# Optimization experiments

Hardware: AMD Instinct MI355X
Metric: run time of the kernel (lower is better)

Reference implementation:

```python
import jax, jax.numpy as jnp
import numpy as np

N, D, K = 131072, 768, 2000


def setup_inputs() -> dict:
    key = jax.random.key(0)
    kx, kc = jax.random.split(key)
    x = jax.random.normal(kx, (N, D), dtype=jnp.float32)
    centroids = jax.random.normal(kc, (D, K), dtype=jnp.float32)  # stored as [D, K] like the torch module
    return {"x": x, "centroids": centroids}


def reference(x, centroids):
    # dist[n,k] = ||x_n||^2 - 2 x_n . c_k + ||c_k||^2  (matmul trick)
    x_norm = jnp.sum(x * x, axis=1, keepdims=True)              # [N, 1]
    c_norm = jnp.sum(centroids * centroids, axis=0, keepdims=True)  # [1, K]
    dist = x_norm - 2.0 * jnp.matmul(x, centroids) + c_norm     # [N, K]
    return jnp.argmin(dist, axis=-1)                            # [N] int
```

## Files before the change

### kernel.cpp

```cpp
#include <hip/hip_runtime.h>
#include <hip/hip_bf16.h>

#define N_ROWS 131072
#define DIM    768
#define K_C    2000
#define K_PAD  2048
#define TAU    0.2f
#define LISTCAP 8192

typedef _Float16 f16;
typedef _Float16 f16x4 __attribute__((ext_vector_type(4)));
typedef _Float16 f16x8 __attribute__((ext_vector_type(8)));
typedef float    f32x4 __attribute__((ext_vector_type(4)));

#define OFF_CN   6291456
#define OFF_XN   6299648
#define OFF_PMIN 6823936
#define OFF_PSEC 15212544
#define OFF_PIDX 23601152
#define OFF_CNT  31989760
#define OFF_LIST 31990016
#define OFF_CN64 32022784
#define OFF_XH   32039168

static __device__ __forceinline__ void gload16(const void* g, void* l) {
  __builtin_amdgcn_global_load_lds(
      (const __attribute__((address_space(1))) unsigned int*)g,
      (__attribute__((address_space(3))) unsigned int*)l, 16, 0, 0);
}

__global__ __launch_bounds__(256) void prep_cn(const float* __restrict__ cent,
                                               float* __restrict__ cn,
                                               double* __restrict__ cn64) {
#pragma clang fp contract(off)
  __shared__ float pf[8][32];
  __shared__ double pd[8][32];
  int t = threadIdx.x;
  int kk = t & 31;
  int k = blockIdx.x * 32 + kk;
  int p = t >> 5;
  float s = 0.0f;
  double s64 = 0.0;
  for (int d = p * 96; d < p * 96 + 96; ++d) {
    float c = (k < K_C) ? cent[d * K_C + k] : 0.0f;
    float sq = c * c;
    s = s + sq;
    s64 += (double)c * (double)c;
  }
  pf[p][kk] = s;
  pd[p][kk] = s64;
  __syncthreads();
  if (p == 0) {
    float ss = 0.0f;
    double ss64 = 0.0;
#pragma unroll
    for (int q = 0; q < 8; ++q) {
      ss = ss + pf[q][kk];
      ss64 += pd[q][kk];
    }
    cn[k] = (k < K_C) ? ss : INFINITY;
    cn64[k] = (k < K_C) ? ss64 : (double)INFINITY;
  }
}

__global__ __launch_bounds__(256) void prep_ct(const float* __restrict__ cent,
                                               f16* __restrict__ cTh) {
  __shared__ float ld[64][65];
  int k0 = blockIdx.x * 64;
  int d0 = blockIdx.y * 64;
  int tid = threadIdx.x;
#pragma unroll
  for (int it = 0; it < 16; ++it) {
    int idx = it * 256 + tid;
    int dd = idx >> 6, kk = idx & 63;
    int k = k0 + kk;
    ld[dd][kk] = (k < K_C) ? cent[(size_t)(d0 + dd) * K_C + k] : 0.0f;
  }
  __syncthreads();
#pragma unroll
  for (int it = 0; it < 16; ++it) {
    int idx = it * 256 + tid;
    int kk = idx >> 6, dd = idx & 63;
    cTh[(size_t)(k0 + kk) * DIM + d0 + dd] = (f16)ld[dd][kk];
  }
}

__global__ __launch_bounds__(256) void xnorm_prepx(const float* __restrict__ x,
                                                   float* __restrict__ xn,
                                                   f16* __restrict__ xh) {
#pragma clang fp contract(off)
  __shared__ __align__(16) float buf[16 * DIM];
  int row0 = blockIdx.x * 16;
  int tid = threadIdx.x;
  const f32x4* src = (const f32x4*)(x + (size_t)row0 * DIM);
  f32x4* dst = (f32x4*)buf;
#pragma unroll
  for (int c = 0; c < 12; ++c) {
    f32x4 v = src[c * 256 + tid];
    dst[c * 256 + tid] = v;
    f16x4 hv;
#pragma unroll
    for (int j = 0; j < 4; ++j) hv[j] = (f16)v[j];
    *(f16x4*)(xh + (size_t)row0 * DIM + (size_t)(c * 256 + tid) * 4) = hv;
  }
  __syncthreads();
  int w = tid >> 6, lane = tid & 63;
  int b = lane >> 3, j = lane & 7;
#pragma unroll
  for (int rr = 0; rr < 4; ++rr) {
    int r = w * 4 + rr;
    const float* a = buf + r * DIM + 96 * b + j;
    float v0 = a[0];
    float acc = v0 * v0;
#pragma unroll
    for (int t = 1; t < 12; ++t) {
      float q = a[8 * t];
      float s = q * q;
      acc = acc + s;
    }
    float v = acc;
    { float o = __shfl_xor(v, 1);  v = v + o; }
    { float o = __shfl_xor(v, 2);  v = v + o; }
    { float o = __shfl_xor(v, 4);  v = v + o; }
    { float o = __shfl_xor(v, 8);  v = v + o; }
    { float o = __shfl_xor(v, 16); v = v + o; }
    { float o = __shfl_xor(v, 32); v = v + o; }
    if (lane == 0) xn[row0 + r] = v;
  }
}

#define STAGE3(bufo)                                                           \
  do {                                                                         \
    gload16(pA0, ldsb + (bufo) + c0 * 1024);                                   \
    gload16(pA1, ldsb + (bufo) + c1 * 1024);                                   \
    gload16(pB0, ldsb + 24576 + (bufo) + c0 * 1024);                           \
    gload16(pB1, ldsb + 24576 + (bufo) + c1 * 1024);                           \
    pA0 += 64; pA1 += 64; pB0 += 64; pB1 += 64;                                \
  } while (0)

__global__ __launch_bounds__(256, 3) void kmeans_main(
    const f16* __restrict__ xh, const f16* __restrict__ cTh,
    const float* __restrict__ cn, const float* __restrict__ xn,
    float* __restrict__ pmin, float* __restrict__ psec,
    int* __restrict__ pidx) {
  __shared__ __align__(16) f16 lds[24576];
  char* ldsb = (char*)lds;

  int d0 = blockIdx.x;
  int g  = (d0 & 7) * 2048 + (d0 >> 3);
  int pb = g & 15;
  int rb = g >> 4;

  int tid  = threadIdx.x;
  int w    = tid >> 6;
  int lane = tid & 63;
  int wrow = (w >> 1) * 64;
  int wcol = (w & 1) * 64;

  int rsel = lane & 15;
  int ksel = lane >> 4;
  int rs = (ksel ^ ((rsel >> 1) & 3)) << 4;

  int c0 = w * 2, c1 = w * 2 + 1;
  int grn = (lane & 3) ^ ((lane >> 3) & 3);
  const char* pA0 = (const char*)xh +
      ((size_t)(rb * 128 + c0 * 16 + (lane >> 2)) * DIM + grn * 8) * 2;
  const char* pA1 = (const char*)xh +
      ((size_t)(rb * 128 + c1 * 16 + (lane >> 2)) * DIM + grn * 8) * 2;
  const char* pB0 = (const char*)cTh +
      ((size_t)(pb * 128 + c0 * 16 + (lane >> 2)) * DIM + grn * 8) * 2;
  const char* pB1 = (const char*)cTh +
      ((size_t)(pb * 128 + c1 * 16 + (lane >> 2)) * DIM + grn * 8) * 2;

  f32x4 acc[4][4] = {};

  STAGE3(0);
  STAGE3(8192);

  int cb = 0;
  int sb = 16384;
#pragma unroll 3
  for (int kt = 0; kt < 24; ++kt) {
    if (kt < 23) {
      asm volatile("s_waitcnt vmcnt(4)" ::: "memory");
    } else {
      asm volatile("s_waitcnt vmcnt(0)" ::: "memory");
    }
    __builtin_amdgcn_sched_barrier(0);
    __builtin_amdgcn_s_barrier();
    __builtin_amdgcn_sched_barrier(0);

    if (kt < 22) STAGE3(sb);

    f16x8 ah[4], bh[4];
    int abase = cb + (wrow + rsel) * 64 + rs;
    int bbase = cb + 24576 + (wcol + rsel) * 64 + rs;
#pragma unroll
    for (int m = 0; m < 4; ++m) ah[m] = *(const f16x8*)(ldsb + abase + m * 1024);
#pragma unroll
    for (int n = 0; n < 4; ++n) bh[n] = *(const f16x8*)(ldsb + bbase + n * 1024);

    __builtin_amdgcn_s_setprio(1);
#pragma unroll
    for (int m = 0; m < 4; ++m)
#pragma unroll
      for (int n = 0; n < 4; ++n)
        acc[m][n] = __builtin_amdgcn_mfma_f32_16x16x32_f16(ah[m], bh[n],
                                                           acc[m][n], 0, 0, 0);
    __builtin_amdgcn_s_setprio(0);

    cb = (cb == 16384) ? 0 : cb + 8192;
    sb = (sb == 16384) ? 0 : sb + 8192;
  }

  __syncthreads();
  float* lv = (float*)lds;
  float* lsv = (float*)lds + 256;
  int*   li = (int*)((float*)lds + 512);

  int colbase = pb * 128 + wcol + rsel;
  float cnv[4];
#pragma unroll
  for (int n = 0; n < 4; ++n) cnv[n] = cn[colbase + n * 16];
  int g4 = ksel * 4;

#pragma unroll
  for (int m = 0; m < 4; ++m) {
#pragma unroll
    for (int j = 0; j < 4; ++j) {
      int trow = wrow + m * 16 + g4 + j;
      float xv = xn[rb * 128 + trow];
      float v1 = 0.0f, v2 = INFINITY;
      int i1 = 0;
#pragma unroll
      for (int n = 0; n < 4; ++n) {
        float dd = (xv - 2.0f * acc[m][n][j]) + cnv[n];
        int ci = colbase + n * 16;
        if (n == 0) { v1 = dd; i1 = ci; }
        else if (dd < v1) { v2 = v1; v1 = dd; i1 = ci; }
        else { v2 = fminf(v2, dd); }
      }
#pragma unroll
      for (int off = 1; off < 16; off <<= 1) {
        float ov1 = __shfl_xor(v1, off);
        float ov2 = __shfl_xor(v2, off);
        int oi1 = __shfl_xor(i1, off);
        if (ov1 < v1 || (ov1 == v1 && oi1 < i1)) {
          v2 = fminf(v1, ov2); v1 = ov1; i1 = oi1;
        } else {
          v2 = fminf(v2, ov1);
        }
      }
      if ((lane & 15) == 0) {
        lv[(w & 1) * 128 + trow] = v1;
        lsv[(w & 1) * 128 + trow] = v2;
        li[(w & 1) * 128 + trow] = i1;
      }
    }
  }
  __syncthreads();
  if (tid < 128) {
    float a1 = lv[tid], a2 = lsv[tid];
    int aj = li[tid];
    float b1 = lv[128 + tid], b2 = lsv[128 + tid];
    int bj = li[128 + tid];
    float v1, v2; int i1;
    if (b1 < a1 || (b1 == a1 && bj < aj)) { v1 = b1; i1 = bj; v2 = fminf(b2, a1); }
    else { v1 = a1; i1 = aj; v2 = fminf(a2, b1); }
    size_t o = (size_t)pb * N_ROWS + rb * 128 + tid;
    pmin[o] = v1;
    psec[o] = v2;
    pidx[o] = i1;
  }
}

__global__ void merge_detect(const float* __restrict__ pmin,
                             const float* __restrict__ psec,
                             const int* __restrict__ pidx, int* __restrict__ out,
                             int* __restrict__ list, int* __restrict__ counter) {
  int n = blockIdx.x * 256 + threadIdx.x;
  float v1 = INFINITY, v2 = INFINITY;
  int i1 = 0x7fffffff;
  for (int p = 0; p < 16; ++p) {
    float a1 = pmin[(size_t)p * N_ROWS + n];
    float a2 = psec[(size_t)p * N_ROWS + n];
    int aj = pidx[(size_t)p * N_ROWS + n];
    if (a1 < v1 || (a1 == v1 && aj < i1)) {
      v2 = fminf(v1, a2); v1 = a1; i1 = aj;
    } else {
      v2 = fminf(v2, a1);
    }
  }
  out[n] = i1;
  if (v2 - v1 < TAU) {
    int idx = atomicAdd(counter, 1);
    if (idx < LISTCAP) list[idx] = n;
  }
}

#define ACCS(R) \
  double a##R##0 = 0, a##R##1 = 0, a##R##2 = 0, a##R##3 = 0, \
         a##R##4 = 0, a##R##5 = 0, a##R##6 = 0, a##R##7 = 0
#define FMAS(R, XV) \
  a##R##0 = fma(XV, c0, a##R##0); a##R##1 = fma(XV, c1, a##R##1); \
  a##R##2 = fma(XV, c2, a##R##2); a##R##3 = fma(XV, c3, a##R##3); \
  a##R##4 = fma(XV, c4, a##R##4); a##R##5 = fma(XV, c5, a##R##5); \
  a##R##6 = fma(XV, c6, a##R##6); a##R##7 = fma(XV, c7, a##R##7)
#define EVAL(R)                                                         \
  {                                                                     \
    double dots[8] = {a##R##0, a##R##1, a##R##2, a##R##3,               \
                      a##R##4, a##R##5, a##R##6, a##R##7};              \
    double bv = (double)INFINITY;                                       \
    int bi = 0x7fffffff;                                                \
    _Pragma("unroll") for (int j = 0; j < 8; ++j) {                     \
      int k = tid + j * 256;                                            \
      if (k < K_C) {                                                    \
        double dd = (xnorms[R] - 2.0 * dots[j]) + cn64[k];              \
        if (dd < bv) { bv = dd; bi = k; }                               \
      }                                                                 \
    }                                                                   \
    rv[tid] = bv; ri[tid] = bi;                                         \
    __syncthreads();                                                    \
    for (int s = 128; s > 0; s >>= 1) {                                 \
      if (tid < s) {                                                    \
        double ov = rv[tid + s];                                        \
        int oi = ri[tid + s];                                           \
        if (ov < rv[tid] || (ov == rv[tid] && oi < ri[tid])) {          \
          rv[tid] = ov; ri[tid] = oi;                                   \
        }                                                               \
      }                                                                 \
      __syncthreads();                                                  \
    }                                                                   \
    if (tid == 0 && (R) < nrows) out[list[b0 + (R)]] = ri[0];           \
    __syncthreads();                                                    \
  }

__global__ __launch_bounds__(256) void exact_recheck64(
    const float* __restrict__ x, const float* __restrict__ cent,
    const double* __restrict__ cn64, const int* __restrict__ list,
    const int* __restrict__ counter, int* __restrict__ out) {
  __shared__ __align__(16) float xrow[4][DIM];
  __shared__ double rv[256];
  __shared__ int ri[256];
  __shared__ double xnorms[4];
  int cnt = counter[0];
  if (cnt > LISTCAP) cnt = LISTCAP;
  int b0 = blockIdx.x * 4;
  if (b0 >= cnt) return;
  int nrows = cnt - b0;
  if (nrows > 4) nrows = 4;
  int tid = threadIdx.x;
  for (int r = 0; r < 4; ++r) {
    int n = list[b0 + (r < nrows ? r : 0)];
    double part = 0.0;
    for (int d = tid; d < DIM; d += 256) {
      float v = x[(size_t)n * DIM + d];
      xrow[r][d] = v;
      part += (double)v * (double)v;
    }
    rv[tid] = part;
    __syncthreads();
    for (int s = 128; s > 0; s >>= 1) {
      if (tid < s) rv[tid] += rv[tid + s];
      __syncthreads();
    }
    if (tid == 0) xnorms[r] = rv[0];
    __syncthreads();
  }

  int k7 = tid + 1792;
  int k7c = (k7 < K_C) ? k7 : (K_C - 1);
  ACCS(0); ACCS(1); ACCS(2); ACCS(3);
#pragma unroll 2
  for (int d = 0; d < DIM; ++d) {
    const float* cp = cent + (size_t)d * K_C + tid;
    double c0 = cp[0], c1 = cp[256], c2 = cp[512], c3 = cp[768];
    double c4 = cp[1024], c5 = cp[1280], c6 = cp[1536];
    double c7 = cp[k7c - tid];
    double x0 = xrow[0][d], x1 = xrow[1][d];
    double x2 = xrow[2][d], x3 = xrow[3][d];
    FMAS(0, x0); FMAS(1, x1); FMAS(2, x2); FMAS(3, x3);
  }
  EVAL(0) EVAL(1) EVAL(2) EVAL(3)
}

extern "C" void kernel_launch(void* const* d_in, const int* in_sizes, int n_in,
                              void* d_out, int out_size, void* d_ws, size_t ws_size,
                              hipStream_t stream) {
  const float* x = (const float*)d_in[0];
  const float* cent = (const float*)d_in[1];
  char* ws = (char*)d_ws;
  f16* cTh = (f16*)ws;
  float* cn = (float*)(ws + OFF_CN);
  float* xn = (float*)(ws + OFF_XN);
  float* pmin = (float*)(ws + OFF_PMIN);
  float* psec = (float*)(ws + OFF_PSEC);
  int* pidx = (int*)(ws + OFF_PIDX);
  int* counter = (int*)(ws + OFF_CNT);
  int* list = (int*)(ws + OFF_LIST);
  double* cn64 = (double*)(ws + OFF_CN64);
  f16* xh = (f16*)(ws + OFF_XH);

  hipMemsetAsync(counter, 0, 4, stream);
  prep_cn<<<64, 256, 0, stream>>>(cent, cn, cn64);
  prep_ct<<<dim3(32, 12), 256, 0, stream>>>(cent, cTh);
  xnorm_prepx<<<N_ROWS / 16, 256, 0, stream>>>(x, xn, xh);
  kmeans_main<<<16384, 256, 0, stream>>>(xh, cTh, cn, xn, pmin, psec, pidx);
  merge_detect<<<N_ROWS / 256, 256, 0, stream>>>(pmin, psec, pidx, (int*)d_out,
                                                 list, counter);
  exact_recheck64<<<LISTCAP / 4, 256, 0, stream>>>(x, cent, cn64, list, counter,
                                                   (int*)d_out);
}
```

Measured before the change: 1.098 ms.

## Widen GEMM block tile to 128x256 with 8x4 MFMA tiles per wave

Each block now computes a 128-row by 256-centroid tile, with every wave covering all 128 rows and its own 64 centroids, in place of a 128x128 tile. This halves the grid and the number of partial-min slabs the merge kernel reads, and raises operand reuse per LDS load. In exchange, per-block LDS and accumulator registers double (launch bounds drop to 2 blocks per CU), which lowers occupancy. The cross-wave merge now drops the index tie-break and uses an odd second-min update.

Result: slower. 1.166 ms (+6.1%).

```diff
diff --git a/kernel.cpp b/kernel.cpp
--- a/kernel.cpp
+++ b/kernel.cpp
@@ -131,58 +131,62 @@
 
 #define STAGE3(bufo)                                                           \
   do {                                                                         \
-    gload16(pA0, ldsb + (bufo) + c0 * 1024);                                   \
-    gload16(pA1, ldsb + (bufo) + c1 * 1024);                                   \
-    gload16(pB0, ldsb + 24576 + (bufo) + c0 * 1024);                           \
-    gload16(pB1, ldsb + 24576 + (bufo) + c1 * 1024);                           \
-    pA0 += 64; pA1 += 64; pB0 += 64; pB1 += 64;                                \
+    gload16(pA0, ldsb + (bufo) + (w * 2) * 1024);                              \
+    gload16(pA1, ldsb + (bufo) + (w * 2 + 1) * 1024);                          \
+    gload16(pB0, ldsb + (bufo) + 8192 + (w * 4) * 1024);                       \
+    gload16(pB1, ldsb + (bufo) + 8192 + (w * 4 + 1) * 1024);                   \
+    gload16(pB2, ldsb + (bufo) + 8192 + (w * 4 + 2) * 1024);                   \
+    gload16(pB3, ldsb + (bufo) + 8192 + (w * 4 + 3) * 1024);                   \
+    pA0 += 64; pA1 += 64; pB0 += 64; pB1 += 64; pB2 += 64; pB3 += 64;          \
   } while (0)
 
-__global__ __launch_bounds__(256, 3) void kmeans_main(
+__global__ __launch_bounds__(256, 2) void kmeans_main(
     const f16* __restrict__ xh, const f16* __restrict__ cTh,
     const float* __restrict__ cn, const float* __restrict__ xn,
     float* __restrict__ pmin, float* __restrict__ psec,
     int* __restrict__ pidx) {
-  __shared__ __align__(16) f16 lds[24576];
+  __shared__ __align__(16) f16 lds[36864];
   char* ldsb = (char*)lds;
 
   int d0 = blockIdx.x;
-  int g  = (d0 & 7) * 2048 + (d0 >> 3);
-  int pb = g & 15;
-  int rb = g >> 4;
+  int g  = (d0 & 7) * 1024 + (d0 >> 3);
+  int pb = g & 7;
+  int rb = g >> 3;
 
   int tid  = threadIdx.x;
   int w    = tid >> 6;
   int lane = tid & 63;
-  int wrow = (w >> 1) * 64;
-  int wcol = (w & 1) * 64;
+  int wcol = w * 64;
 
   int rsel = lane & 15;
   int ksel = lane >> 4;
   int rs = (ksel ^ ((rsel >> 1) & 3)) << 4;
 
-  int c0 = w * 2, c1 = w * 2 + 1;
   int grn = (lane & 3) ^ ((lane >> 3) & 3);
   const char* pA0 = (const char*)xh +
-      ((size_t)(rb * 128 + c0 * 16 + (lane >> 2)) * DIM + grn * 8) * 2;
+      ((size_t)(rb * 128 + (w * 2) * 16 + (lane >> 2)) * DIM + grn * 8) * 2;
   const char* pA1 = (const char*)xh +
-      ((size_t)(rb * 128 + c1 * 16 + (lane >> 2)) * DIM + grn * 8) * 2;
+      ((size_t)(rb * 128 + (w * 2 + 1) * 16 + (lane >> 2)) * DIM + grn * 8) * 2;
   const char* pB0 = (const char*)cTh +
-      ((size_t)(pb * 128 + c0 * 16 + (lane >> 2)) * DIM + grn * 8) * 2;
+      ((size_t)(pb * 256 + (w * 4) * 16 + (lane >> 2)) * DIM + grn * 8) * 2;
   const char* pB1 = (const char*)cTh +
-      ((size_t)(pb * 128 + c1 * 16 + (lane >> 2)) * DIM + grn * 8) * 2;
-
-  f32x4 acc[4][4] = {};
+      ((size_t)(pb * 256 + (w * 4 + 1) * 16 + (lane >> 2)) * DIM + grn * 8) * 2;
+  const char* pB2 = (const char*)cTh +
+      ((size_t)(pb * 256 + (w * 4 + 2) * 16 + (lane >> 2)) * DIM + grn * 8) * 2;
+  const char* pB3 = (const char*)cTh +
+      ((size_t)(pb * 256 + (w * 4 + 3) * 16 + (lane >> 2)) * DIM + grn * 8) * 2;
+
+  f32x4 acc[8][4] = {};
 
   STAGE3(0);
-  STAGE3(8192);
+  STAGE3(24576);
 
   int cb = 0;
-  int sb = 16384;
+  int sb = 49152;
 #pragma unroll 3
   for (int kt = 0; kt < 24; ++kt) {
     if (kt < 23) {
-      asm volatile("s_waitcnt vmcnt(4)" ::: "memory");
+      asm volatile("s_waitcnt vmcnt(6)" ::: "memory");
     } else {
       asm volatile("s_waitcnt vmcnt(0)" ::: "memory");
     }
@@ -192,43 +196,43 @@
 
     if (kt < 22) STAGE3(sb);
 
-    f16x8 ah[4], bh[4];
-    int abase = cb + (wrow + rsel) * 64 + rs;
-    int bbase = cb + 24576 + (wcol + rsel) * 64 + rs;
-#pragma unroll
-    for (int m = 0; m < 4; ++m) ah[m] = *(const f16x8*)(ldsb + abase + m * 1024);
+    f16x8 ah[8], bh[4];
+    int abase = cb + rsel * 64 + rs;
+    int bbase = cb + 8192 + (wcol + rsel) * 64 + rs;
+#pragma unroll
+    for (int m = 0; m < 8; ++m) ah[m] = *(const f16x8*)(ldsb + abase + m * 1024);
 #pragma unroll
     for (int n = 0; n < 4; ++n) bh[n] = *(const f16x8*)(ldsb + bbase + n * 1024);
 
     __builtin_amdgcn_s_setprio(1);
 #pragma unroll
-    for (int m = 0; m < 4; ++m)
+    for (int m = 0; m < 8; ++m)
 #pragma unroll
       for (int n = 0; n < 4; ++n)
         acc[m][n] = __builtin_amdgcn_mfma_f32_16x16x32_f16(ah[m], bh[n],
                                                            acc[m][n], 0, 0, 0);
     __builtin_amdgcn_s_setprio(0);
 
-    cb = (cb == 16384) ? 0 : cb + 8192;
-    sb = (sb == 16384) ? 0 : sb + 8192;
+    cb = (cb == 49152) ? 0 : cb + 24576;
+    sb = (sb == 49152) ? 0 : sb + 24576;
   }
 
   __syncthreads();
   float* lv = (float*)lds;
-  float* lsv = (float*)lds + 256;
-  int*   li = (int*)((float*)lds + 512);
-
-  int colbase = pb * 128 + wcol + rsel;
+  float* lsv = (float*)lds + 512;
+  int*   li = (int*)((float*)lds + 1024);
+
+  int colbase = pb * 256 + wcol + rsel;
   float cnv[4];
 #pragma unroll
   for (int n = 0; n < 4; ++n) cnv[n] = cn[colbase + n * 16];
   int g4 = ksel * 4;
 
 #pragma unroll
-  for (int m = 0; m < 4; ++m) {
+  for (int m = 0; m < 8; ++m) {
 #pragma unroll
     for (int j = 0; j < 4; ++j) {
-      int trow = wrow + m * 16 + g4 + j;
+      int trow = m * 16 + g4 + j;
       float xv = xn[rb * 128 + trow];
       float v1 = 0.0f, v2 = INFINITY;
       int i1 = 0;
@@ -252,21 +256,28 @@
         }
       }
       if ((lane & 15) == 0) {
-        lv[(w & 1) * 128 + trow] = v1;
-        lsv[(w & 1) * 128 + trow] = v2;
-        li[(w & 1) * 128 + trow] = i1;
+        lv[w * 128 + trow] = v1;
+        lsv[w * 128 + trow] = v2;
+        li[w * 128 + trow] = i1;
       }
     }
   }
   __syncthreads();
   if (tid < 128) {
-    float a1 = lv[tid], a2 = lsv[tid];
-    int aj = li[tid];
-    float b1 = lv[128 + tid], b2 = lsv[128 + tid];
-    int bj = li[128 + tid];
-    float v1, v2; int i1;
-    if (b1 < a1 || (b1 == a1 && bj < aj)) { v1 = b1; i1 = bj; v2 = fminf(b2, a1); }
-    else { v1 = a1; i1 = aj; v2 = fminf(a2, b1); }
+    float v1 = lv[tid], v2 = lsv[tid];
+    int i1 = li[tid];
+#pragma unroll
+    for (int q = 1; q < 4; ++q) {
+      float b1 = lv[q * 128 + tid], b2 = lsv[q * 128 + tid];
+      int bj = li[q * 128 + tid];
+      if (b1 < v1) {
+        v2 = fminf(v1, b2);
+        v1 = b1; i1 = bj;
+      } else {
+        v2 = fminf(v2, fminf(b1, b2) == b1 ? b1 : b1);
+        v2 = fminf(v2, b2 < b1 ? b2 : b1);
+      }
+    }
     size_t o = (size_t)pb * N_ROWS + rb * 128 + tid;
     pmin[o] = v1;
     psec[o] = v2;
@@ -281,7 +292,7 @@
   int n = blockIdx.x * 256 + threadIdx.x;
   float v1 = INFINITY, v2 = INFINITY;
   int i1 = 0x7fffffff;
-  for (int p = 0; p < 16; ++p) {
+  for (int p = 0; p < 8; ++p) {
     float a1 = pmin[(size_t)p * N_ROWS + n];
     float a2 = psec[(size_t)p * N_ROWS + n];
     int aj = pidx[(size_t)p * N_ROWS + n];
@@ -405,7 +416,7 @@
   prep_cn<<<64, 256, 0, stream>>>(cent, cn, cn64);
   prep_ct<<<dim3(32, 12), 256, 0, stream>>>(cent, cTh);
   xnorm_prepx<<<N_ROWS / 16, 256, 0, stream>>>(x, xn, xh);
-  kmeans_main<<<16384, 256, 0, stream>>>(xh, cTh, cn, xn, pmin, psec, pidx);
+  kmeans_main<<<8192, 256, 0, stream>>>(xh, cTh, cn, xn, pmin, psec, pidx);
   merge_detect<<<N_ROWS / 256, 256, 0, stream>>>(pmin, psec, pidx, (int*)d_out,
                                                  list, counter);
   exact_recheck64<<<LISTCAP / 4, 256, 0, stream>>>(x, cent, cn64, list, counter,
```
